# Performance work log

Hardware: AMD Instinct MI355X
Metric: run time of the kernel (lower is better)

Reference implementation:

```python
import jax, jax.numpy as jnp
import numpy as np

N_NODES, D = 10000, 128
N_EDGES = 640000
BN_EPS = 1e-3  # keras BatchNormalization default


def _bn(x, gamma, beta, mean, var):
    return (x - mean) * jax.lax.rsqrt(var + BN_EPS) * gamma + beta


def _ffn_block(x, gamma, beta, mean, var, W, b):
    # BatchNorm (inference) -> Dropout (identity at inference) -> Dense + gelu (exact, keras default)
    return jax.nn.gelu(_bn(x, gamma, beta, mean, var) @ W + b, approximate=False)


def setup_inputs() -> dict:
    key = jax.random.key(0)
    ks = jax.random.split(key, 32)
    inp = {
        "node_features": jax.random.normal(ks[0], (N_NODES, D), jnp.float32),
        "edges": jax.random.randint(ks[1], (2, N_EDGES), 0, N_NODES, jnp.int64),
        "edge_weights": jax.random.uniform(ks[2], (N_EDGES,), jnp.float32),
    }
    def bn_params(i, dim, prefix):
        return {
            prefix + "_g": jnp.ones((dim,), jnp.float32) + 0.1 * jax.random.normal(ks[i], (dim,)),
            prefix + "_b": 0.1 * jax.random.normal(ks[i + 1], (dim,)),
            prefix + "_m": 0.1 * jax.random.normal(ks[i + 2], (dim,)),
            prefix + "_v": jax.random.uniform(ks[i + 3], (dim,), minval=0.5, maxval=1.5),
        }
    def dense_params(i, din, dout, prefix):
        s = (2.0 / (din + dout)) ** 0.5
        return {
            prefix + "_W": s * jax.random.normal(ks[i], (din, dout), jnp.float32),
            prefix + "_bias": jnp.zeros((dout,), jnp.float32),
        }
    # prepare FFN: BN(D)->Dense(D->128), BN(128)->Dense(128->128)
    inp.update(bn_params(3, D, "p1")); inp.update(dense_params(7, D, 128, "p1"))
    inp.update(bn_params(8, 128, "p2")); inp.update(dense_params(12, 128, 128, "p2"))
    # update FFN (concat -> 2*D input): BN(2D)->Dense(2D->128), BN(128)->Dense(128->128)
    inp.update(bn_params(13, 2 * D, "u1")); inp.update(dense_params(17, 2 * D, 128, "u1"))
    inp.update(bn_params(18, 128, "u2")); inp.update(dense_params(22, 128, 128, "u2"))
    return inp


def reference(node_features, edges, edge_weights,
              p1_g, p1_b, p1_m, p1_v, p1_W, p1_bias,
              p2_g, p2_b, p2_m, p2_v, p2_W, p2_bias,
              u1_g, u1_b, u1_m, u1_v, u1_W, u1_bias,
              u2_g, u2_b, u2_m, u2_v, u2_W, u2_bias):
    num_nodes = node_features.shape[0]
    node_idx, nbr_idx = edges[0], edges[1]
    # gather neighbor representations [E, D]
    neigh = node_features[nbr_idx]
    # prepare: ffn on neighbors, then scale by edge weights
    msg = _ffn_block(neigh, p1_g, p1_b, p1_m, p1_v, p1_W, p1_bias)
    msg = _ffn_block(msg, p2_g, p2_b, p2_m, p2_v, p2_W, p2_bias)
    msg = msg * edge_weights[:, None]
    # aggregate: unsorted_segment_mean
    agg = jax.ops.segment_sum(msg, node_idx, num_segments=num_nodes)
    cnt = jax.ops.segment_sum(jnp.ones_like(edge_weights), node_idx, num_segments=num_nodes)
    agg = agg / jnp.maximum(cnt, 1.0)[:, None]
    # update: concat + ffn
    h = jnp.concatenate([node_features, agg], axis=1)
    h = _ffn_block(h, u1_g, u1_b, u1_m, u1_v, u1_W, u1_bias)
    h = _ffn_block(h, u2_g, u2_b, u2_m, u2_v, u2_W, u2_bias)
    return h
```

## Files before the change

kernel.cpp:

```cpp
#include <hip/hip_runtime.h>
#include <hip/hip_bf16.h>
#include <hip/hip_fp16.h>
#include <math.h>

#define N_NODES 10000
#define DIM 128
#define N_EDGES 640000
#define BN_EPS 1e-3f

#define QUARTER 2500
#define PART_BLOCKS 250
#define EDGES_PER_PART 2560
#define SCAT_GRID 1000
#define MSG64_BLOCKS 157
#define SU_BLOCKS 1250
#define HIST_PAD 10240

typedef _Float16 half8 __attribute__((ext_vector_type(8)));
typedef float f32x4 __attribute__((ext_vector_type(4)));

__device__ __forceinline__ float gelu_exact(float x) {
  return 0.5f * x * (1.0f + erff(x * 0.70710678f));
}

__device__ __forceinline__ int lds_swz(int row, int colbyte) {
  return ((row * 256 + colbyte) ^ ((row & 7) << 4));
}

struct FoldAll {
  const float* g[4];
  const float* bb[4];
  const float* m[4];
  const float* v[4];
  const float* W[4];
  const float* bias[4];
  _Float16* pk[4];
  float* bf[4];
  int din[4];
  int S[4];
};

__global__ __launch_bounds__(256) void fold_hist_kernel(FoldAll fa,
                                                        const int* __restrict__ node_idx,
                                                        unsigned char* __restrict__ part) {
  __shared__ int lh[N_NODES];
  __shared__ float t_sh[256];
  __shared__ float bpart[128];
  int b = blockIdx.x, t = threadIdx.x;
  if (b >= 44) {
    int eb = b - 44;
    for (int i = t; i < N_NODES; i += 256) lh[i] = 0;
    __syncthreads();
    int base0 = eb * EDGES_PER_PART;
#pragma unroll
    for (int s = 0; s < 3; ++s) {
      int off = s * 1024 + t * 4;
      if (off < EDGES_PER_PART) {
        int4 vv = *reinterpret_cast<const int4*>(&node_idx[base0 + off]);
        atomicAdd(&lh[vv.x], 1);
        atomicAdd(&lh[vv.y], 1);
        atomicAdd(&lh[vv.z], 1);
        atomicAdd(&lh[vv.w], 1);
      }
    }
    __syncthreads();
    for (int i = t; i < N_NODES; i += 256) {
      int q = i / QUARTER;
      int bp = i - q * QUARTER;
      part[(size_t)(q * PART_BLOCKS + eb) * QUARTER + bp] = (unsigned char)lh[i];
    }
    return;
  }
  if (b >= 40) {
    int p = b - 40;
    int din = fa.din[p];
    const float* W = fa.W[p];
    for (int k = t; k < din; k += 256) {
      float sc = fa.g[p][k] * rsqrtf(fa.v[p][k] + BN_EPS);
      t_sh[k] = fa.bb[p][k] - fa.m[p][k] * sc;
    }
    __syncthreads();
    int j = t & 127, kh = t >> 7;
    int half = din >> 1;
    float acc = 0.f;
    for (int k = kh * half; k < (kh + 1) * half; ++k)
      acc = fmaf(t_sh[k], W[k * 128 + j], acc);
    if (kh == 1) bpart[j] = acc;
    __syncthreads();
    if (kh == 0) fa.bf[p][j] = acc + bpart[j] + fa.bias[p][j];
    return;
  }
  int p, lf;
  if (b < 8)       { p = 0; lf = b * 256 + t; }
  else if (b < 16) { p = 1; lf = (b - 8) * 256 + t; }
  else if (b < 32) { p = 2; lf = (b - 16) * 256 + t; }
  else             { p = 3; lf = (b - 32) * 256 + t; }
  int S = fa.S[p];
  int l = lf & 63;
  int fs = lf >> 6;
  int f = fs & 7, s = fs >> 3;
  if (s >= S) return;
  const float* W = fa.W[p];
  const float* g = fa.g[p];
  const float* v = fa.v[p];
  int k0 = s * 32 + (l >> 4) * 8;
  int col = f * 16 + (l & 15);
  half8 h;
#pragma unroll
  for (int i = 0; i < 8; ++i) {
    int k = k0 + i;
    float sc = g[k] * rsqrtf(v[k] + BN_EPS);
    h[i] = (_Float16)(sc * W[k * 128 + col]);
  }
  *reinterpret_cast<half8*>(fa.pk[p] + (size_t)lf * 8) = h;
}

__global__ __launch_bounds__(256) void merge_msg_kernel(
    unsigned char* __restrict__ part, int* __restrict__ hist,
    const float* __restrict__ x,
    const _Float16* __restrict__ W1pk, const float* __restrict__ b1f,
    const _Float16* __restrict__ W2pk, const float* __restrict__ b2f,
    _Float16* __restrict__ M) {
  __shared__ char lds_raw[4 * 4096];
  int b = blockIdx.x, t = threadIdx.x;
  if (b < 40) {
    int bin = b * 256 + t;
    if (bin < N_NODES) {
      int q = bin / QUARTER;
      int bp = bin - q * QUARTER;
      unsigned char* col = part + (size_t)q * PART_BLOCKS * QUARTER + bp;
      int sum = 0;
#pragma unroll
      for (int c = 0; c < PART_BLOCKS; c += 25) {
        int vals[25];
#pragma unroll
        for (int i = 0; i < 25; ++i) vals[i] = col[(size_t)(c + i) * QUARTER];
#pragma unroll
        for (int i = 0; i < 25; ++i) {
          col[(size_t)(c + i) * QUARTER] = (unsigned char)sum;
          sum += vals[i];
        }
      }
      hist[bin] = sum;
    } else if (bin < HIST_PAD) {
      hist[bin] = 0;
    }
    return;
  }
  int wid = t >> 6, lane = t & 63;
  int r = lane & 15, g = lane >> 4;
  int row0 = (b - 40) * 64 + wid * 16;
  char* lbase = lds_raw + wid * 4096;

  int arow = row0 + r;
  if (arow > N_NODES - 1) arow = N_NODES - 1;
  const float* xp = x + (size_t)arow * DIM;

  half8 a[4];
#pragma unroll
  for (int s = 0; s < 4; ++s) {
    float4 lo = *reinterpret_cast<const float4*>(xp + s * 32 + g * 8);
    float4 hi = *reinterpret_cast<const float4*>(xp + s * 32 + g * 8 + 4);
    half8 h;
    h[0] = (_Float16)lo.x; h[1] = (_Float16)lo.y; h[2] = (_Float16)lo.z; h[3] = (_Float16)lo.w;
    h[4] = (_Float16)hi.x; h[5] = (_Float16)hi.y; h[6] = (_Float16)hi.z; h[7] = (_Float16)hi.w;
    a[s] = h;
  }

  f32x4 zero = {0.f, 0.f, 0.f, 0.f};
  f32x4 acc[8];
#pragma unroll
  for (int f = 0; f < 8; ++f) acc[f] = zero;
#pragma unroll
  for (int f = 0; f < 8; ++f)
#pragma unroll
    for (int s = 0; s < 4; ++s) {
      half8 bfrag = *reinterpret_cast<const half8*>(W1pk + (size_t)((s * 8 + f) * 64 + lane) * 8);
      acc[f] = __builtin_amdgcn_mfma_f32_16x16x32_f16(a[s], bfrag, acc[f], 0, 0, 0);
    }

#pragma unroll
  for (int f = 0; f < 8; ++f) {
    int col = f * 16 + r;
    float bv = b1f[col];
#pragma unroll
    for (int j = 0; j < 4; ++j) {
      int rl = g * 4 + j;
      float gv = gelu_exact(acc[f][j] + bv);
      *reinterpret_cast<_Float16*>(lbase + lds_swz(rl, col * 2)) = (_Float16)gv;
    }
  }

  half8 a2[4];
#pragma unroll
  for (int s = 0; s < 4; ++s)
    a2[s] = *reinterpret_cast<const half8*>(lbase + lds_swz(r, (s * 32 + g * 8) * 2));

  f32x4 acc2[8];
#pragma unroll
  for (int f = 0; f < 8; ++f) acc2[f] = zero;
#pragma unroll
  for (int f = 0; f < 8; ++f)
#pragma unroll
    for (int s = 0; s < 4; ++s) {
      half8 bfrag = *reinterpret_cast<const half8*>(W2pk + (size_t)((s * 8 + f) * 64 + lane) * 8);
      acc2[f] = __builtin_amdgcn_mfma_f32_16x16x32_f16(a2[s], bfrag, acc2[f], 0, 0, 0);
    }

#pragma unroll
  for (int f = 0; f < 8; ++f) {
    int col = f * 16 + r;
    float bv = b2f[col];
#pragma unroll
    for (int j = 0; j < 4; ++j) {
      int grow = row0 + g * 4 + j;
      if (grow < N_NODES)
        M[(size_t)grow * DIM + col] = (_Float16)gelu_exact(acc2[f][j] + bv);
    }
  }
}

__global__ __launch_bounds__(256) void scatter_kernel(
    const int* __restrict__ node_idx, const int* __restrict__ nbr_idx,
    const float* __restrict__ ew, const int* __restrict__ hist,
    const unsigned char* __restrict__ part, uint2* __restrict__ edge_s,
    int* __restrict__ row_start) {
  __shared__ int cur[QUARTER];
  __shared__ int sums[256];
  int bk = blockIdx.x, t = threadIdx.x;
  int eb = bk >> 2;
  int q = bk & 3;
  int qbase = q * QUARTER;
  const int PER = 40;
  int i0 = t * PER;
  int lh[PER];
  int total = 0;
#pragma unroll
  for (int i = 0; i < PER; i += 4) {
    int4 h4 = *reinterpret_cast<const int4*>(&hist[i0 + i]);
    lh[i] = h4.x; lh[i + 1] = h4.y; lh[i + 2] = h4.z; lh[i + 3] = h4.w;
    total += h4.x + h4.y + h4.z + h4.w;
  }
  sums[t] = total;
  __syncthreads();
  for (int off = 1; off < 256; off <<= 1) {
    int v = (t >= off) ? sums[t - off] : 0;
    __syncthreads();
    sums[t] += v;
    __syncthreads();
  }
  int running = sums[t] - total;
  const unsigned char* prow = part + (size_t)(q * PART_BLOCKS + eb) * QUARTER;
  bool wrs = (bk == 0);
#pragma unroll
  for (int i = 0; i < PER; ++i) {
    int idx = i0 + i;
    if (idx < N_NODES) {
      unsigned d = (unsigned)(idx - qbase);
      if (d < QUARTER) cur[d] = running + (int)prow[d];
      if (wrs) row_start[idx] = running;
      running += lh[i];
    }
  }
  if (wrs && t == 255) row_start[N_NODES] = running;
  __syncthreads();

  int base0 = eb * EDGES_PER_PART;
#pragma unroll
  for (int s = 0; s < 3; ++s) {
    int off = s * 1024 + t * 4;
    if (off >= EDGES_PER_PART) break;
    int base = base0 + off;
    int4 ni = *reinterpret_cast<const int4*>(&node_idx[base]);
    int4 nb = *reinterpret_cast<const int4*>(&nbr_idx[base]);
    float4 wv = *reinterpret_cast<const float4*>(&ew[base]);
    unsigned d0 = (unsigned)(ni.x - qbase);
    unsigned d1 = (unsigned)(ni.y - qbase);
    unsigned d2 = (unsigned)(ni.z - qbase);
    unsigned d3 = (unsigned)(ni.w - qbase);
    if (d0 < QUARTER) {
      int p0 = atomicAdd(&cur[d0], 1);
      edge_s[p0] = make_uint2((unsigned)nb.x, __float_as_uint(wv.x));
    }
    if (d1 < QUARTER) {
      int p1 = atomicAdd(&cur[d1], 1);
      edge_s[p1] = make_uint2((unsigned)nb.y, __float_as_uint(wv.y));
    }
    if (d2 < QUARTER) {
      int p2 = atomicAdd(&cur[d2], 1);
      edge_s[p2] = make_uint2((unsigned)nb.z, __float_as_uint(wv.z));
    }
    if (d3 < QUARTER) {
      int p3 = atomicAdd(&cur[d3], 1);
      edge_s[p3] = make_uint2((unsigned)nb.w, __float_as_uint(wv.w));
    }
  }
}

__global__ __launch_bounds__(256) void spmm_update_kernel(
    const int* __restrict__ row_start, const uint2* __restrict__ edge_s,
    const __half* __restrict__ M, const float* __restrict__ x,
    const _Float16* __restrict__ U1pk, const float* __restrict__ bu1,
    const _Float16* __restrict__ U2pk, const float* __restrict__ bu2,
    float* __restrict__ out) {
  __shared__ float scratch[3][8][128];
  __shared__ char tile[4096];
  int t = threadIdx.x;
  int row0 = blockIdx.x * 8;

  {
    int r = t >> 5;
    int q = t & 31;
    int slice = q >> 3;
    int sub = q & 7;
    int row = row0 + r;
    int s = row_start[row];
    int e_end = row_start[row + 1];
    float acc[16];
#pragma unroll
    for (int c = 0; c < 16; ++c) acc[c] = 0.f;
    const __half* Mb = M + sub * 16;
    for (int base = s + slice * 4; base < e_end; base += 16) {
      uint2 pk[4];
#pragma unroll
      for (int k = 0; k < 4; ++k) {
        int e = base + k;
        pk[k] = edge_s[(e < e_end) ? e : s];
        if (e >= e_end) pk[k].y = 0u;
      }
      uint4 raw[8];
#pragma unroll
      for (int k = 0; k < 4; ++k) {
        const uint4* mp = reinterpret_cast<const uint4*>(Mb + (size_t)pk[k].x * DIM);
        raw[2 * k] = mp[0];
        raw[2 * k + 1] = mp[1];
      }
#pragma unroll
      for (int k = 0; k < 4; ++k) {
        float w = __uint_as_float(pk[k].y);
        const __half2* h2 = reinterpret_cast<const __half2*>(&raw[2 * k]);
#pragma unroll
        for (int qq = 0; qq < 8; ++qq) {
          float2 f = __half22float2(h2[qq]);
          acc[2 * qq] = fmaf(w, f.x, acc[2 * qq]);
          acc[2 * qq + 1] = fmaf(w, f.y, acc[2 * qq + 1]);
        }
      }
    }
    if (slice >= 1) {
      float* dst = &scratch[slice - 1][r][sub * 16];
      *reinterpret_cast<float4*>(dst) = make_float4(acc[0], acc[1], acc[2], acc[3]);
      *reinterpret_cast<float4*>(dst + 4) = make_float4(acc[4], acc[5], acc[6], acc[7]);
      *reinterpret_cast<float4*>(dst + 8) = make_float4(acc[8], acc[9], acc[10], acc[11]);
      *reinterpret_cast<float4*>(dst + 12) = make_float4(acc[12], acc[13], acc[14], acc[15]);
    }
    __syncthreads();
    if (slice == 0) {
#pragma unroll
      for (int sl = 0; sl < 3; ++sl) {
        const float* src = &scratch[sl][r][sub * 16];
#pragma unroll
        for (int c = 0; c < 16; c += 4) {
          float4 o = *reinterpret_cast<const float4*>(src + c);
          acc[c] += o.x; acc[c + 1] += o.y; acc[c + 2] += o.z; acc[c + 3] += o.w;
        }
      }
      int cnt = e_end - s;
      float inv = 1.f / (float)(cnt > 0 ? cnt : 1);
      half8 hlo, hhi;
#pragma unroll
      for (int c = 0; c < 8; ++c) hlo[c] = (_Float16)(acc[c] * inv);
#pragma unroll
      for (int c = 0; c < 8; ++c) hhi[c] = (_Float16)(acc[8 + c] * inv);
      *reinterpret_cast<half8*>(tile + lds_swz(r, sub * 32)) = hlo;
      *reinterpret_cast<half8*>(tile + lds_swz(r, sub * 32 + 16)) = hhi;
    }
  }
  __syncthreads();

  int wid = t >> 6, lane = t & 63;
  int r = lane & 15, g = lane >> 4;
  half8 hzero;
#pragma unroll
  for (int i = 0; i < 8; ++i) hzero[i] = (_Float16)0.f;

  half8 a[8];
#pragma unroll
  for (int s = 0; s < 8; ++s) a[s] = hzero;
  if (r < 8) {
    const float* xp = x + (size_t)(row0 + r) * DIM;
#pragma unroll
    for (int s = 0; s < 4; ++s) {
      float4 lo = *reinterpret_cast<const float4*>(xp + s * 32 + g * 8);
      float4 hi = *reinterpret_cast<const float4*>(xp + s * 32 + g * 8 + 4);
      half8 h;
      h[0] = (_Float16)lo.x; h[1] = (_Float16)lo.y; h[2] = (_Float16)lo.z; h[3] = (_Float16)lo.w;
      h[4] = (_Float16)hi.x; h[5] = (_Float16)hi.y; h[6] = (_Float16)hi.z; h[7] = (_Float16)hi.w;
      a[s] = h;
    }
#pragma unroll
    for (int s = 0; s < 4; ++s)
      a[4 + s] = *reinterpret_cast<const half8*>(tile + lds_swz(r, (s * 32 + g * 8) * 2));
  }
  __syncthreads();

  f32x4 zero = {0.f, 0.f, 0.f, 0.f};
  {
    f32x4 acc1[2];
    acc1[0] = zero; acc1[1] = zero;
#pragma unroll
    for (int fi = 0; fi < 2; ++fi) {
      int f = wid * 2 + fi;
#pragma unroll
      for (int s = 0; s < 8; ++s) {
        half8 bfrag = *reinterpret_cast<const half8*>(U1pk + (size_t)((s * 8 + f) * 64 + lane) * 8);
        acc1[fi] = __builtin_amdgcn_mfma_f32_16x16x32_f16(a[s], bfrag, acc1[fi], 0, 0, 0);
      }
    }
#pragma unroll
    for (int fi = 0; fi < 2; ++fi) {
      int f = wid * 2 + fi;
      int col = f * 16 + r;
      float bv = bu1[col];
#pragma unroll
      for (int j = 0; j < 4; ++j) {
        int rl = g * 4 + j;
        float gv = gelu_exact(acc1[fi][j] + bv);
        *reinterpret_cast<_Float16*>(tile + lds_swz(rl, col * 2)) = (_Float16)gv;
      }
    }
  }
  __syncthreads();

  {
    half8 a2[4];
#pragma unroll
    for (int s = 0; s < 4; ++s) a2[s] = hzero;
    if (r < 8) {
#pragma unroll
      for (int s = 0; s < 4; ++s)
        a2[s] = *reinterpret_cast<const half8*>(tile + lds_swz(r, (s * 32 + g * 8) * 2));
    }
    f32x4 acc2[2];
    acc2[0] = zero; acc2[1] = zero;
#pragma unroll
    for (int fi = 0; fi < 2; ++fi) {
      int f = wid * 2 + fi;
#pragma unroll
      for (int s = 0; s < 4; ++s) {
        half8 bfrag = *reinterpret_cast<const half8*>(U2pk + (size_t)((s * 8 + f) * 64 + lane) * 8);
        acc2[fi] = __builtin_amdgcn_mfma_f32_16x16x32_f16(a2[s], bfrag, acc2[fi], 0, 0, 0);
      }
    }
#pragma unroll
    for (int fi = 0; fi < 2; ++fi) {
      int f = wid * 2 + fi;
      int col = f * 16 + r;
      float bv = bu2[col];
#pragma unroll
      for (int j = 0; j < 4; ++j) {
        int rloc = g * 4 + j;
        if (rloc < 8)
          out[(size_t)(row0 + rloc) * DIM + col] = gelu_exact(acc2[fi][j] + bv);
      }
    }
  }
}

extern "C" void kernel_launch(void* const* d_in, const int* in_sizes, int n_in,
                              void* d_out, int out_size, void* d_ws, size_t ws_size,
                              hipStream_t stream) {
  const float* x = (const float*)d_in[0];
  const int* edges = (const int*)d_in[1];
  const float* ew = (const float*)d_in[2];

  const int* node_idx = edges;
  const int* nbr_idx = edges + N_EDGES;

  char* wsp = (char*)d_ws;
  auto alloc = [&](size_t bytes) {
    char* p = wsp;
    wsp += (bytes + 255) & ~(size_t)255;
    return p;
  };
  _Float16* M = (_Float16*)alloc((size_t)N_NODES * DIM * 2);
  _Float16* W1pk = (_Float16*)alloc(128 * 128 * 2);
  _Float16* W2pk = (_Float16*)alloc(128 * 128 * 2);
  _Float16* U1pk = (_Float16*)alloc(256 * 128 * 2);
  _Float16* U2pk = (_Float16*)alloc(128 * 128 * 2);
  float* b1f = (float*)alloc(128 * 4);
  float* b2f = (float*)alloc(128 * 4);
  float* bu1 = (float*)alloc(128 * 4);
  float* bu2 = (float*)alloc(128 * 4);
  int* hist = (int*)alloc(HIST_PAD * 4);
  int* row_start = (int*)alloc((N_NODES + 1) * 4);
  unsigned char* part = (unsigned char*)alloc((size_t)PART_BLOCKS * N_NODES);
  uint2* edge_s = (uint2*)alloc((size_t)N_EDGES * 8);

  FoldAll fa;
  fa.g[0] = (const float*)d_in[3];  fa.bb[0] = (const float*)d_in[4];
  fa.m[0] = (const float*)d_in[5];  fa.v[0] = (const float*)d_in[6];
  fa.W[0] = (const float*)d_in[7];  fa.bias[0] = (const float*)d_in[8];
  fa.g[1] = (const float*)d_in[9];  fa.bb[1] = (const float*)d_in[10];
  fa.m[1] = (const float*)d_in[11]; fa.v[1] = (const float*)d_in[12];
  fa.W[1] = (const float*)d_in[13]; fa.bias[1] = (const float*)d_in[14];
  fa.g[2] = (const float*)d_in[15]; fa.bb[2] = (const float*)d_in[16];
  fa.m[2] = (const float*)d_in[17]; fa.v[2] = (const float*)d_in[18];
  fa.W[2] = (const float*)d_in[19]; fa.bias[2] = (const float*)d_in[20];
  fa.g[3] = (const float*)d_in[21]; fa.bb[3] = (const float*)d_in[22];
  fa.m[3] = (const float*)d_in[23]; fa.v[3] = (const float*)d_in[24];
  fa.W[3] = (const float*)d_in[25]; fa.bias[3] = (const float*)d_in[26];
  fa.pk[0] = W1pk; fa.pk[1] = W2pk; fa.pk[2] = U1pk; fa.pk[3] = U2pk;
  fa.bf[0] = b1f; fa.bf[1] = b2f; fa.bf[2] = bu1; fa.bf[3] = bu2;
  fa.din[0] = 128; fa.din[1] = 128; fa.din[2] = 256; fa.din[3] = 128;
  fa.S[0] = 4; fa.S[1] = 4; fa.S[2] = 8; fa.S[3] = 4;

  fold_hist_kernel<<<44 + PART_BLOCKS, 256, 0, stream>>>(fa, node_idx, part);
  merge_msg_kernel<<<40 + MSG64_BLOCKS, 256, 0, stream>>>(
      part, hist, x, W1pk, b1f, W2pk, b2f, M);
  scatter_kernel<<<SCAT_GRID, 256, 0, stream>>>(
      node_idx, nbr_idx, ew, hist, part, edge_s, row_start);
  spmm_update_kernel<<<SU_BLOCKS, 256, 0, stream>>>(
      row_start, edge_s, (const __half*)M, x, U1pk, bu1, U2pk, bu2, (float*)d_out);
}
```

Before: 108.1 us.

## Use per-quarter histograms with global quarter totals and prefetch edge records in SpMM

```diff
diff --git a/kernel.cpp b/kernel.cpp
--- a/kernel.cpp
+++ b/kernel.cpp
@@ -9,12 +9,12 @@
 #define BN_EPS 1e-3f
 
 #define QUARTER 2500
+#define QPAD 3072
 #define PART_BLOCKS 250
 #define EDGES_PER_PART 2560
 #define SCAT_GRID 1000
 #define MSG64_BLOCKS 157
 #define SU_BLOCKS 1250
-#define HIST_PAD 10240
 
 typedef _Float16 half8 __attribute__((ext_vector_type(8)));
 typedef float f32x4 __attribute__((ext_vector_type(4)));
@@ -42,7 +42,9 @@
 
 __global__ __launch_bounds__(256) void fold_hist_kernel(FoldAll fa,
                                                         const int* __restrict__ node_idx,
-                                                        unsigned char* __restrict__ part) {
+                                                        unsigned char* __restrict__ part,
+                                                        int* __restrict__ histq,
+                                                        int* __restrict__ qtot) {
   __shared__ int lh[N_NODES];
   __shared__ float t_sh[256];
   __shared__ float bpart[128];
@@ -73,6 +75,8 @@
   }
   if (b >= 40) {
     int p = b - 40;
+    if (p == 0 && t < 4) qtot[t] = 0;
+    for (int i = t; i < QPAD - QUARTER; i += 256) histq[p * QPAD + QUARTER + i] = 0;
     int din = fa.din[p];
     const float* W = fa.W[p];
     for (int k = t; k < din; k += 256) {
@@ -116,20 +120,23 @@
 }
 
 __global__ __launch_bounds__(256) void merge_msg_kernel(
-    unsigned char* __restrict__ part, int* __restrict__ hist,
+    unsigned char* __restrict__ part, int* __restrict__ histq,
+    int* __restrict__ qtot,
     const float* __restrict__ x,
     const _Float16* __restrict__ W1pk, const float* __restrict__ b1f,
     const _Float16* __restrict__ W2pk, const float* __restrict__ b2f,
     _Float16* __restrict__ M) {
   __shared__ char lds_raw[4 * 4096];
+  __shared__ int qsum[4];
   int b = blockIdx.x, t = threadIdx.x;
   if (b < 40) {
     int bin = b * 256 + t;
+    int sum = 0;
+    int q = 0;
     if (bin < N_NODES) {
-      int q = bin / QUARTER;
+      q = bin / QUARTER;
       int bp = bin - q * QUARTER;
       unsigned char* col = part + (size_t)q * PART_BLOCKS * QUARTER + bp;
-      int sum = 0;
 #pragma unroll
       for (int c = 0; c < PART_BLOCKS; c += 25) {
         int vals[25];
@@ -141,10 +148,13 @@
           sum += vals[i];
         }
       }
-      hist[bin] = sum;
-    } else if (bin < HIST_PAD) {
-      hist[bin] = 0;
-    }
+      histq[q * QPAD + bp] = sum;
+    }
+    if (t < 4) qsum[t] = 0;
+    __syncthreads();
+    if (bin < N_NODES) atomicAdd(&qsum[q], sum);
+    __syncthreads();
+    if (t < 4) atomicAdd(&qtot[t], qsum[t]);
     return;
   }
   int wid = t >> 6, lane = t & 63;
@@ -222,7 +232,8 @@
 
 __global__ __launch_bounds__(256) void scatter_kernel(
     const int* __restrict__ node_idx, const int* __restrict__ nbr_idx,
-    const float* __restrict__ ew, const int* __restrict__ hist,
+    const float* __restrict__ ew, const int* __restrict__ histq,
+    const int* __restrict__ qtot,
     const unsigned char* __restrict__ part, uint2* __restrict__ edge_s,
     int* __restrict__ row_start) {
   __shared__ int cur[QUARTER];
@@ -231,13 +242,14 @@
   int eb = bk >> 2;
   int q = bk & 3;
   int qbase = q * QUARTER;
-  const int PER = 40;
+  const int PER = 12;
   int i0 = t * PER;
+  const int* hq = histq + q * QPAD;
   int lh[PER];
   int total = 0;
 #pragma unroll
   for (int i = 0; i < PER; i += 4) {
-    int4 h4 = *reinterpret_cast<const int4*>(&hist[i0 + i]);
+    int4 h4 = *reinterpret_cast<const int4*>(&hq[i0 + i]);
     lh[i] = h4.x; lh[i + 1] = h4.y; lh[i + 2] = h4.z; lh[i + 3] = h4.w;
     total += h4.x + h4.y + h4.z + h4.w;
   }
@@ -249,20 +261,21 @@
     sums[t] += v;
     __syncthreads();
   }
-  int running = sums[t] - total;
+  int q0 = qtot[0], q1 = qtot[1], q2 = qtot[2];
+  int qpre = (q >= 1 ? q0 : 0) + (q >= 2 ? q1 : 0) + (q >= 3 ? q2 : 0);
+  int running = qpre + sums[t] - total;
   const unsigned char* prow = part + (size_t)(q * PART_BLOCKS + eb) * QUARTER;
-  bool wrs = (bk == 0);
+  bool wrs = (eb == 0);
 #pragma unroll
   for (int i = 0; i < PER; ++i) {
     int idx = i0 + i;
-    if (idx < N_NODES) {
-      unsigned d = (unsigned)(idx - qbase);
-      if (d < QUARTER) cur[d] = running + (int)prow[d];
-      if (wrs) row_start[idx] = running;
+    if (idx < QUARTER) {
+      cur[idx] = running + (int)prow[idx];
+      if (wrs) row_start[qbase + idx] = running;
       running += lh[i];
     }
   }
-  if (wrs && t == 255) row_start[N_NODES] = running;
+  if (bk == 0 && t == 0) row_start[N_NODES] = N_EDGES;
   __syncthreads();
 
   int base0 = eb * EDGES_PER_PART;
@@ -320,13 +333,22 @@
 #pragma unroll
     for (int c = 0; c < 16; ++c) acc[c] = 0.f;
     const __half* Mb = M + sub * 16;
-    for (int base = s + slice * 4; base < e_end; base += 16) {
-      uint2 pk[4];
+    int base = s + slice * 4;
+    uint2 pk[4];
+#pragma unroll
+    for (int k = 0; k < 4; ++k) {
+      int e = base + k;
+      pk[k] = edge_s[(e < e_end) ? e : s];
+      if (e >= e_end) pk[k].y = 0u;
+    }
+    for (; base < e_end; base += 16) {
+      uint2 pkn[4];
+      int nb = base + 16;
 #pragma unroll
       for (int k = 0; k < 4; ++k) {
-        int e = base + k;
-        pk[k] = edge_s[(e < e_end) ? e : s];
-        if (e >= e_end) pk[k].y = 0u;
+        int e = nb + k;
+        pkn[k] = edge_s[(e < e_end) ? e : s];
+        if (e >= e_end) pkn[k].y = 0u;
       }
       uint4 raw[8];
 #pragma unroll
@@ -346,6 +368,8 @@
           acc[2 * qq + 1] = fmaf(w, f.y, acc[2 * qq + 1]);
         }
       }
+#pragma unroll
+      for (int k = 0; k < 4; ++k) pk[k] = pkn[k];
     }
     if (slice >= 1) {
       float* dst = &scratch[slice - 1][r][sub * 16];
@@ -492,7 +516,8 @@
   float* b2f = (float*)alloc(128 * 4);
   float* bu1 = (float*)alloc(128 * 4);
   float* bu2 = (float*)alloc(128 * 4);
-  int* hist = (int*)alloc(HIST_PAD * 4);
+  int* histq = (int*)alloc(4 * QPAD * 4);
+  int* qtot = (int*)alloc(4 * 4);
   int* row_start = (int*)alloc((N_NODES + 1) * 4);
   unsigned char* part = (unsigned char*)alloc((size_t)PART_BLOCKS * N_NODES);
   uint2* edge_s = (uint2*)alloc((size_t)N_EDGES * 8);
@@ -515,11 +540,11 @@
   fa.din[0] = 128; fa.din[1] = 128; fa.din[2] = 256; fa.din[3] = 128;
   fa.S[0] = 4; fa.S[1] = 4; fa.S[2] = 8; fa.S[3] = 4;
 
-  fold_hist_kernel<<<44 + PART_BLOCKS, 256, 0, stream>>>(fa, node_idx, part);
+  fold_hist_kernel<<<44 + PART_BLOCKS, 256, 0, stream>>>(fa, node_idx, part, histq, qtot);
   merge_msg_kernel<<<40 + MSG64_BLOCKS, 256, 0, stream>>>(
-      part, hist, x, W1pk, b1f, W2pk, b2f, M);
+      part, histq, qtot, x, W1pk, b1f, W2pk, b2f, M);
   scatter_kernel<<<SCAT_GRID, 256, 0, stream>>>(
-      node_idx, nbr_idx, ew, hist, part, edge_s, row_start);
+      node_idx, nbr_idx, ew, histq, qtot, part, edge_s, row_start);
   spmm_update_kernel<<<SU_BLOCKS, 256, 0, stream>>>(
       row_start, edge_s, (const __half*)M, x, U1pk, bu1, U2pk, bu2, (float*)d_out);
 }
```

New measurement: 105.3 us. 1.03x faster.
